# Performance work log

Measured on AMD Instinct MI355X. Metric: run time of the kernel, lower is better.

## Reference

```python
import jax, jax.numpy as jnp
import numpy as np
import math

B, T, C_EMB, H, M, P = 4, 8192, 1024, 16, 64, 8
D = C_EMB // H
L = int(math.log2(T // M)) - 1  # = 6 levels of coarse attention
SCALE_ATTN = True
NEG = -1e30


def setup_inputs() -> dict:
    key = jax.random.key(0)
    ks = jax.random.split(key, 4)
    x = jax.random.normal(ks[0], (B, T, C_EMB), jnp.float32)
    W_attn = jax.random.normal(ks[1], (C_EMB, 3 * C_EMB), jnp.float32) * (1.0 / math.sqrt(C_EMB))
    b_attn = jnp.zeros((3 * C_EMB,), jnp.float32)
    W_proj = jax.random.normal(ks[2], (C_EMB, C_EMB), jnp.float32) * (1.0 / math.sqrt(C_EMB))
    b_proj = jnp.zeros((C_EMB,), jnp.float32)
    return {"x": x, "W_attn": W_attn, "b_attn": b_attn, "W_proj": W_proj, "b_proj": b_proj}


def _shift(t, s):
    # shift blocks forward along axis 1 by s, zero-padding at the front
    pad = jnp.zeros_like(t[:, :s])
    return jnp.concatenate([pad, t[:, :-s]], axis=1)


def _fma_attention(q, k, v):
    # q, k, v: [BH, T, D]; q already scaled by 1/sqrt(D)
    BH = q.shape[0]
    # --- convolute(): avgpool downsampled K, V at each level ---
    Kls, Vls = [k], [v]
    for l in range(L):
        r = (M * 2 ** l) // P  # pool kernel = stride
        Kls.append(k.reshape(BH, T // r, r, D).mean(axis=2))
        Vls.append(v.reshape(BH, T // r, r, D).mean(axis=2))
    # --- stage1: banded QK at every level ---
    As = []
    # fine level 0: causal sliding window of M keys (j in [i-M+1, i])
    nb0 = T // M
    qb = q.reshape(BH, nb0, M, D)
    kb = k.reshape(BH, nb0, M, D)
    s_prev = jnp.einsum('bgqd,bgkd->bgqk', qb, _shift(kb, 1))
    s_self = jnp.einsum('bgqd,bgkd->bgqk', qb, kb)
    r_idx = jnp.arange(M)[:, None]
    c_idx = jnp.arange(M)[None, :]
    g_ok = (jnp.arange(nb0) >= 1)[None, :, None, None]
    s_prev = jnp.where((c_idx > r_idx) & g_ok, s_prev, NEG)
    s_self = jnp.where(c_idx <= r_idx, s_self, NEG)
    As.append(jnp.concatenate([s_prev, s_self], axis=-1).reshape(BH, T, 2 * M))
    # coarse levels l=1..L: query block (width w) attends to the P summaries of
    # each of the two preceding coarse blocks (causal, left-to-right)
    for l in range(1, L + 1):
        w = M * 2 ** (l - 1)
        nb = T // w
        qw = q.reshape(BH, nb, w, D)
        kc = Kls[l].reshape(BH, nb, P, D)
        scores = []
        for s in (2, 1):
            sc = jnp.einsum('bgqd,bgpd->bgqp', qw, _shift(kc, s))
            ok = (jnp.arange(nb) >= s)[None, :, None, None]
            scores.append(jnp.where(ok, sc, NEG))
        As.append(jnp.concatenate(scores, axis=-1).reshape(BH, T, 2 * P))
    # --- fused multi-level softmax (shared max + shared normalizer) ---
    gmax = jnp.max(jnp.stack([a.max(axis=-1) for a in As], axis=-1), axis=-1)  # [BH, T]
    Es = [jnp.exp(a - gmax[..., None]) for a in As]
    scales = [1] + [((M * 2 ** (l - 1)) // P if SCALE_ATTN else 1) for l in range(1, L + 1)]
    denom = sum(float(s) * e.sum(axis=-1) for s, e in zip(scales, Es))[..., None]
    Cs = [float(s) * e / denom for s, e in zip(scales, Es)]
    # --- stage2: banded CV ---
    vb = v.reshape(BH, nb0, M, D)
    C0 = Cs[0].reshape(BH, nb0, M, 2 * M)
    out = (jnp.einsum('bgqk,bgkd->bgqd', C0[..., :M], _shift(vb, 1)) +
           jnp.einsum('bgqk,bgkd->bgqd', C0[..., M:], vb)).reshape(BH, T, D)
    for l in range(1, L + 1):
        w = M * 2 ** (l - 1)
        nb = T // w
        vc = Vls[l].reshape(BH, nb, P, D)
        Cl = Cs[l].reshape(BH, nb, w, 2 * P)
        ol = (jnp.einsum('bgqp,bgpd->bgqd', Cl[..., :P], _shift(vc, 2)) +
              jnp.einsum('bgqp,bgpd->bgqd', Cl[..., P:], _shift(vc, 1)))
        out = out + ol.reshape(BH, T, D)
    return out


def reference(x, W_attn, b_attn, W_proj, b_proj):
    Bx, Tx, Cx = x.shape
    qkv = x @ W_attn + b_attn
    q, k, v = jnp.split(qkv, 3, axis=-1)

    def heads(t):
        return t.reshape(Bx, Tx, H, D).transpose(0, 2, 1, 3).reshape(Bx * H, Tx, D)

    q = heads(q) / math.sqrt(D)
    o = _fma_attention(q, heads(k), heads(v))
    o = o.reshape(Bx, H, Tx, D).transpose(0, 2, 1, 3).reshape(Bx, Tx, Cx)
    return o @ W_proj + b_proj
```

## Files before the change

### kernel.cpp

```cpp
#include <hip/hip_runtime.h>
#include <hip/hip_bf16.h>
#include <stdint.h>


typedef float  f32x4  __attribute__((ext_vector_type(4)));
typedef __bf16 bf16x8 __attribute__((ext_vector_type(8)));
typedef unsigned short ushort8 __attribute__((ext_vector_type(8)));
typedef unsigned short ushort4v __attribute__((ext_vector_type(4)));
typedef unsigned uint4v __attribute__((ext_vector_type(4)));

__device__ __forceinline__ unsigned short f2bf(float f) {
  union { float f; unsigned u; } v; v.f = f;
  unsigned r = v.u + 0x7fffu + ((v.u >> 16) & 1u);
  return (unsigned short)(r >> 16);
}
__device__ __forceinline__ float bf2f(unsigned short s) {
  union { unsigned u; float f; } v; v.u = ((unsigned)s) << 16;
  return v.f;
}
__device__ __forceinline__ bf16x8 ld_bf8(const unsigned short* p) {
  return __builtin_bit_cast(bf16x8, *(const ushort8*)p);
}
__device__ __forceinline__ f32x4 mfma16(bf16x8 a, bf16x8 b, f32x4 c) {
  return __builtin_amdgcn_mfma_f32_16x16x32_bf16(a, b, c, 0, 0, 0);
}
__device__ __forceinline__ f32x4 zero4() {
  f32x4 z; z[0] = 0.f; z[1] = 0.f; z[2] = 0.f; z[3] = 0.f; return z;
}
__device__ __forceinline__ void gload16(const void* g, void* lds) {
  __builtin_amdgcn_global_load_lds(
      (const __attribute__((address_space(1))) void*)(uintptr_t)g,
      (__attribute__((address_space(3))) void*)(unsigned int)(uintptr_t)lds,
      16, 0, 0);
}

#define T_SEQ 8192
#define NPOOL 2016

#define SCHED0() __builtin_amdgcn_sched_barrier(0)
#define VMC(n)                                           \
  do {                                                   \
    SCHED0();                                            \
    asm volatile("s_waitcnt vmcnt(" #n ")" ::: "memory");\
    SCHED0();                                            \
  } while (0)

__global__ __launch_bounds__(256) void castx_k(const float* __restrict__ x,
                                               unsigned short* __restrict__ xb) {
  size_t i = ((size_t)blockIdx.x * 256 + threadIdx.x) * 8;
  float4 a = *(const float4*)(x + i);
  float4 b = *(const float4*)(x + i + 4);
  ushort8 o;
  o[0] = f2bf(a.x); o[1] = f2bf(a.y); o[2] = f2bf(a.z); o[3] = f2bf(a.w);
  o[4] = f2bf(b.x); o[5] = f2bf(b.y); o[6] = f2bf(b.z); o[7] = f2bf(b.w);
  *(ushort8*)(xb + i) = o;
}

__global__ __launch_bounds__(256) void transposeW_k(const float* __restrict__ w,
                                                    unsigned short* __restrict__ wt,
                                                    int R, int C) {
  __shared__ float tile[64 * 65];
  int cc = blockIdx.x, rc = blockIdx.y;
  int tid = threadIdx.x;
#pragma unroll
  for (int p = 0; p < 4; ++p) {
    int ci = p * 256 + tid;
    int r = ci >> 4, q4 = ci & 15;
    float4 v = *(const float4*)(w + (size_t)(rc * 64 + r) * C + cc * 64 + q4 * 4);
    tile[r * 65 + q4 * 4 + 0] = v.x;
    tile[r * 65 + q4 * 4 + 1] = v.y;
    tile[r * 65 + q4 * 4 + 2] = v.z;
    tile[r * 65 + q4 * 4 + 3] = v.w;
  }
  __syncthreads();
#pragma unroll
  for (int p = 0; p < 2; ++p) {
    int orow = p * 32 + (tid >> 3), tg = tid & 7;
    ushort8 ov;
#pragma unroll
    for (int i = 0; i < 8; ++i) ov[i] = f2bf(tile[(tg * 8 + i) * 65 + orow]);
    *(ushort8*)(wt + (size_t)(cc * 64 + orow) * R + rc * 64 + tg * 8) = ov;
  }
}

template<int NTILE_N, int EPI>
__global__ __launch_bounds__(512, 2) void gemm256(
    const unsigned short* __restrict__ A, const unsigned short* __restrict__ Bt,
    const float* __restrict__ bias,
    unsigned short* __restrict__ o0, unsigned short* __restrict__ o1,
    unsigned short* __restrict__ o2, float* __restrict__ fout) {
  extern __shared__ __align__(16) char smem[];
  const int K = 1024;
  const int nwg = 128 * NTILE_N;
  const int q = nwg >> 3;
  const int wg = ((int)blockIdx.x & 7) * q + ((int)blockIdx.x >> 3);
  const int tm = wg & 127, tn = wg >> 7;
  const int tid = threadIdx.x;
  const int wid = tid >> 6, lane = tid & 63;
  const int wm = wid >> 2, wn = wid & 3;
  const int lr = lane & 15, lg = lane >> 4;

  const int srow = tid >> 2;
  const int sseg = (tid & 3) ^ ((tid >> 3) & 3);
  const unsigned short* aSrc = A + (size_t)(tm * 256 + srow) * K + sseg * 8;
  const unsigned short* bSrc = Bt + (size_t)(tn * 256 + srow) * K + sseg * 8;
  const unsigned ldsT = (unsigned)tid * 16;

  const unsigned psel = (unsigned)((lg ^ ((lr >> 1) & 3)) * 16);
  const unsigned aBase = (unsigned)(wm * 8192 + lr * 64) + psel;
  const unsigned bBase = (unsigned)(16384 + wn * 4096 + lr * 64) + psel;

  f32x4 acc[8][4];
#pragma unroll
  for (int i = 0; i < 8; ++i)
#pragma unroll
    for (int j = 0; j < 4; ++j) acc[i][j] = zero4();

  bf16x8 rA0[4], rA1[4], rB0[4], rB1[4];

  auto SB = [&]() {
    SCHED0();
    __builtin_amdgcn_s_barrier();
    SCHED0();
  };
  auto stage2 = [&](int coffShorts, unsigned slotB) {
#pragma unroll
    for (int pass = 0; pass < 2; ++pass) {
      gload16(aSrc + (size_t)pass * 128 * K + coffShorts,
              smem + slotB + pass * 8192 + ldsT);
      gload16(bSrc + (size_t)pass * 128 * K + coffShorts,
              smem + slotB + 16384 + pass * 8192 + ldsT);
    }
  };
  auto rdA = [&](bf16x8 (&dst)[4], unsigned slotB, int ih) {
    const char* p = smem + slotB + aBase + ih * 4096;
#pragma unroll
    for (int ii = 0; ii < 4; ++ii)
      dst[ii] = ld_bf8((const unsigned short*)(p + ii * 1024));
  };
  auto rdB = [&](bf16x8 (&dst)[4], unsigned slotB) {
    const char* p = smem + slotB + bBase;
#pragma unroll
    for (int j = 0; j < 4; ++j)
      dst[j] = ld_bf8((const unsigned short*)(p + j * 1024));
  };
  auto cluster = [&](int rb, bf16x8 (&a)[4], bf16x8 (&b)[4]) {
    __builtin_amdgcn_s_setprio(1);
#pragma unroll
    for (int ii = 0; ii < 4; ++ii)
#pragma unroll
      for (int j = 0; j < 4; ++j)
        acc[rb + ii][j] = mfma16(b[j], a[ii], acc[rb + ii][j]);
    __builtin_amdgcn_s_setprio(0);
  };

  stage2(0, 0u);
  stage2(32, 32768u);
  stage2(64, 65536u);
  stage2(96, 98304u);
  VMC(12);
  SB();
  rdA(rA0, 0u, 0);
  rdB(rB0, 0u);

  for (int t = 0; t < 16; ++t) {
    const unsigned s0  = (unsigned)((2 * t) & 3) * 32768u;
    const unsigned s1  = (unsigned)((2 * t + 1) & 3) * 32768u;
    const unsigned sn0 = (unsigned)((2 * t + 2) & 3) * 32768u;
    rdA(rA1, s0, 1);
    if (t < 15) { VMC(8); } else { VMC(0); }
    SB();
    cluster(0, rA0, rB0);
    if (t < 14) stage2((t + 2) * 64, s0);
    rdA(rA0, s1, 0);
    rdB(rB1, s1);
    SB();
    cluster(4, rA1, rB0);
    rdA(rA1, s1, 1);
    if (t < 14) { VMC(8); } else if (t == 14) { VMC(4); }
    SB();
    cluster(0, rA0, rB1);
    if (t < 14) stage2((t + 2) * 64 + 32, s1);
    if (t < 15) { rdA(rA0, sn0, 0); rdB(rB0, sn0); }
    SB();
    cluster(4, rA1, rB1);
  }

  const int mBase = tm * 256 + wm * 128;
  const int nBase = tn * 256 + wn * 64;
  if (EPI == 0) {
    const int region = nBase >> 10, nn = nBase & 1023, hh = nn >> 6;
    unsigned short* dst = region == 0 ? o0 : (region == 1 ? o1 : o2);
#pragma unroll
    for (int j = 0; j < 4; ++j) {
      const int d0 = (nn & 63) + j * 16 + lg * 4;
      const float4 bv = *(const float4*)(bias + nBase + j * 16 + lg * 4);
#pragma unroll
      for (int i = 0; i < 8; ++i) {
        const int m = mBase + i * 16 + lr;
        const int bb = m >> 13, tq = m & 8191;
        ushort4v pk;
        pk[0] = f2bf(acc[i][j][0] + bv.x);
        pk[1] = f2bf(acc[i][j][1] + bv.y);
        pk[2] = f2bf(acc[i][j][2] + bv.z);
        pk[3] = f2bf(acc[i][j][3] + bv.w);
        *(ushort4v*)(dst + (((size_t)(bb * 16 + hh)) * T_SEQ + tq) * 64 + d0) = pk;
      }
    }
  } else {
#pragma unroll
    for (int j = 0; j < 4; ++j) {
      const int n0 = nBase + j * 16 + lg * 4;
      const float4 bv = *(const float4*)(bias + n0);
#pragma unroll
      for (int i = 0; i < 8; ++i) {
        const int m = mBase + i * 16 + lr;
        float4 ov;
        ov.x = acc[i][j][0] + bv.x;
        ov.y = acc[i][j][1] + bv.y;
        ov.z = acc[i][j][2] + bv.z;
        ov.w = acc[i][j][3] + bv.w;
        *(float4*)(fout + (size_t)m * 1024 + n0) = ov;
      }
    }
  }
}

__global__ __launch_bounds__(256) void transposeV_k(const unsigned short* __restrict__ v,
                                                    unsigned short* __restrict__ vt) {
  __shared__ float tile[64 * 65];
  int tc = blockIdx.x, bh = blockIdx.y;
  int tid = threadIdx.x;
#pragma unroll
  for (int p = 0; p < 2; ++p) {
    int r = p * 32 + (tid >> 3), cg = tid & 7;
    ushort8 u = *(const ushort8*)(v + ((size_t)bh * T_SEQ + (size_t)tc * 64 + r) * 64 + cg * 8);
#pragma unroll
    for (int i = 0; i < 8; ++i) tile[r * 65 + cg * 8 + i] = bf2f(u[i]);
  }
  __syncthreads();
#pragma unroll
  for (int p = 0; p < 2; ++p) {
    int dd = p * 32 + (tid >> 3), tg = tid & 7;
    ushort8 ov;
#pragma unroll
    for (int i = 0; i < 8; ++i) ov[i] = f2bf(tile[(tg * 8 + i) * 65 + dd]);
    *(ushort8*)(vt + ((size_t)bh * 64 + dd) * T_SEQ + (size_t)tc * 64 + tg * 8) = ov;
  }
}

__global__ __launch_bounds__(256) void poolK_k(const unsigned short* __restrict__ kin,
                                               unsigned short* __restrict__ kpool) {
  __shared__ float buf[64 * 65];
  int chunk = blockIdx.x, bh = blockIdx.y;
  int tid = threadIdx.x;
  int cg = tid & 7, orow = tid >> 3;
  float s[8];
#pragma unroll
  for (int i = 0; i < 8; ++i) s[i] = 0.f;
  const unsigned short* base =
      kin + ((size_t)bh * T_SEQ + chunk * 256 + orow * 8) * 64 + cg * 8;
#pragma unroll
  for (int rr = 0; rr < 8; ++rr) {
    ushort8 v = *(const ushort8*)(base + (size_t)rr * 64);
#pragma unroll
    for (int i = 0; i < 8; ++i) s[i] += bf2f(v[i]);
  }
  unsigned short* kp = kpool + (size_t)bh * NPOOL * 64;
  {
    ushort8 ov;
#pragma unroll
    for (int i = 0; i < 8; ++i) {
      s[i] *= 0.125f;
      ov[i] = f2bf(s[i]);
      buf[orow * 65 + cg * 8 + i] = s[i];
    }
    *(ushort8*)(kp + ((size_t)(chunk * 32 + orow)) * 64 + cg * 8) = ov;
  }
  __syncthreads();
  int srcR = 0, dstR = 32;
#pragma unroll
  for (int lvl = 2; lvl <= 6; ++lvl) {
    int rows = 32 >> (lvl - 1);
    int off = 2048 - (2048 >> (lvl - 1));
    if (orow < rows) {
      ushort8 ov;
      float tv[8];
#pragma unroll
      for (int i = 0; i < 8; ++i) {
        tv[i] = 0.5f * (buf[(srcR + 2 * orow) * 65 + cg * 8 + i] +
                        buf[(srcR + 2 * orow + 1) * 65 + cg * 8 + i]);
        ov[i] = f2bf(tv[i]);
      }
      *(ushort8*)(kp + ((size_t)(off + chunk * rows + orow)) * 64 + cg * 8) = ov;
#pragma unroll
      for (int i = 0; i < 8; ++i) buf[(dstR + orow) * 65 + cg * 8 + i] = tv[i];
    }
    __syncthreads();
    srcR = dstR;
    dstR += rows;
  }
}

__global__ __launch_bounds__(256) void poolV_k(const unsigned short* __restrict__ vt,
                                               unsigned short* __restrict__ vtpool) {
  __shared__ float buf[1024 + 512 + 256 + 128 + 64];
  int d = blockIdx.x, bh = blockIdx.y;
  int tid = threadIdx.x;
  const unsigned short* src = vt + ((size_t)bh * 64 + d) * T_SEQ;
  unsigned short* dst = vtpool + ((size_t)bh * 64 + d) * NPOOL;
#pragma unroll
  for (int p = 0; p < 4; ++p) {
    int oi = p * 256 + tid;
    ushort8 v = *(const ushort8*)(src + (size_t)oi * 8);
    float s = 0.f;
#pragma unroll
    for (int i = 0; i < 8; ++i) s += bf2f(v[i]);
    s *= 0.125f;
    dst[oi] = f2bf(s);
    buf[oi] = s;
  }
  __syncthreads();
  float* b1 = buf; float* b2 = buf + 1024;
#pragma unroll
  for (int p = 0; p < 2; ++p) {
    int oi = p * 256 + tid;
    float s = 0.5f * (b1[2 * oi] + b1[2 * oi + 1]);
    dst[1024 + oi] = f2bf(s);
    b2[oi] = s;
  }
  __syncthreads();
  float* b3 = b2 + 512;
  {
    float s = 0.5f * (b2[2 * tid] + b2[2 * tid + 1]);
    dst[1536 + tid] = f2bf(s);
    b3[tid] = s;
  }
  __syncthreads();
  float* b4 = b3 + 256;
  if (tid < 128) {
    float s = 0.5f * (b3[2 * tid] + b3[2 * tid + 1]);
    dst[1792 + tid] = f2bf(s);
    b4[tid] = s;
  }
  __syncthreads();
  float* b5 = b4 + 128;
  if (tid < 64) {
    float s = 0.5f * (b4[2 * tid] + b4[2 * tid + 1]);
    dst[1920 + tid] = f2bf(s);
    b5[tid] = s;
  }
  __syncthreads();
  if (tid < 32) {
    float s = 0.5f * (b5[2 * tid] + b5[2 * tid + 1]);
    dst[1984 + tid] = f2bf(s);
  }
}

__global__ __launch_bounds__(256) void attn_k(const unsigned short* __restrict__ q,
                                              const unsigned short* __restrict__ k,
                                              const unsigned short* __restrict__ kpool,
                                              const unsigned short* __restrict__ vt,
                                              const unsigned short* __restrict__ vtpool,
                                              unsigned short* __restrict__ o) {
  const int g = blockIdx.x;
  const int bh = blockIdx.y;
  const int tid = threadIdx.x;
  const int w = tid >> 6, l = tid & 63;
  const int lr = l & 15, lg = l >> 4;
  __shared__ unsigned short KV[224 * 64];

  const size_t qoff = ((size_t)bh * T_SEQ + (size_t)g * 64 + w * 16 + lr) * 64 + lg * 8;
  bf16x8 aq0 = ld_bf8(q + qoff);
  bf16x8 aq1 = ld_bf8(q + qoff + 32);
  SCHED0();

  const int krow = tid >> 3;
  const int kseg = tid & 7;
#pragma unroll
  for (int p = 0; p < 7; ++p) {
    const int row = p * 32 + krow;
    const unsigned short* src;
    if (row < 128) {
      int t0 = (g - 1) * 64 + row;
      if (t0 < 0) t0 = 0;
      src = k + ((size_t)bh * T_SEQ + t0) * 64;
    } else {
      const int pr = row - 128;
      const int lvl0 = pr >> 4;
      const int off = 2048 - (2048 >> lvl0);
      const int gl = g >> lvl0;
      int st = (gl - 2) * 8 + (pr & 15);
      if (st < 0) st = 0;
      src = kpool + ((size_t)bh * NPOOL + off + st) * 64;
    }
    gload16(src + (kseg ^ (row & 7)) * 8,
            ((char*)KV) + p * 4096 + (unsigned)tid * 16);
  }
  SCHED0();

  const int vr = tid >> 2;
  const int vg = tid & 3;
  const int vswz = vg ^ ((vr >> 1) & 3);
  ushort8 vstg[7];
#pragma unroll
  for (int s = 0; s < 7; ++s) {
    const int colsh = s * 32 + vswz * 8;
    const unsigned short* src;
    if (colsh < 128) {
      int t0 = (g - 1) * 64 + colsh;
      if (t0 < 0) t0 = 0;
      src = vt + ((size_t)bh * 64 + vr) * T_SEQ + t0;
    } else {
      const int c = colsh - 128;
      const int lvl = c >> 4;
      const int off = 2048 - (2048 >> lvl);
      const int gl = g >> lvl;
      int start = (gl - 2) * 8 + (c & 15);
      if (start < 0) start = 0;
      src = vtpool + ((size_t)bh * 64 + vr) * NPOOL + off + start;
    }
    vstg[s] = *(const ushort8*)src;
  }
  SCHED0();
  asm volatile("s_waitcnt vmcnt(7)" ::: "memory");
  SCHED0();
  __builtin_amdgcn_s_barrier();
  SCHED0();

  f32x4 S[14];
#pragma unroll
  for (int ct = 0; ct < 14; ++ct) S[ct] = zero4();
#pragma unroll
  for (int ct = 0; ct < 14; ++ct) {
    const int row = ct * 16 + lr;
    const unsigned short* kr = KV + row * 64;
    const int sw = row & 7;
    S[ct] = mfma16(ld_bf8(kr + (lg ^ sw) * 8), aq0, S[ct]);
    S[ct] = mfma16(ld_bf8(kr + ((lg + 4) ^ sw) * 8), aq1, S[ct]);
  }
  SCHED0();
  __builtin_amdgcn_s_barrier();
  SCHED0();

#pragma unroll
  for (int s = 0; s < 7; ++s)
    *(ushort8*)&KV[s * 2048 + vr * 32 + vg * 8] = vstg[s];

  const float NEGF = -1e30f;
  const int qq = w * 16 + lr;
#pragma unroll
  for (int ct = 0; ct < 14; ++ct) {
#pragma unroll
    for (int e = 0; e < 4; ++e) {
      float s = S[ct][e] * 0.125f;
      bool valid;
      if (ct < 8) {
        int kk = ct * 16 + lg * 4 + e;
        valid = (kk > qq) && (kk <= qq + 64) && ((g >= 1) || (kk >= 64));
      } else {
        int lvl = ct - 7;
        int gl = g >> (lvl - 1);
        valid = gl >= ((lg < 2) ? 2 : 1);
      }
      S[ct][e] = valid ? s : NEGF;
    }
  }
  float mx = S[0][0];
#pragma unroll
  for (int ct = 0; ct < 14; ++ct)
#pragma unroll
    for (int e = 0; e < 4; ++e) mx = fmaxf(mx, S[ct][e]);
  mx = fmaxf(mx, __shfl_xor(mx, 16));
  mx = fmaxf(mx, __shfl_xor(mx, 32));
  float sum = 0.f;
#pragma unroll
  for (int ct = 0; ct < 14; ++ct) {
    const float sc = (ct < 8) ? 1.0f : (float)(8 << (ct - 8));
#pragma unroll
    for (int e = 0; e < 4; ++e) {
      float ev = sc * __expf(S[ct][e] - mx);
      S[ct][e] = ev;
      sum += ev;
    }
  }
  sum += __shfl_xor(sum, 16);
  sum += __shfl_xor(sum, 32);
  const float invd = 1.0f / sum;

  unsigned pw[14][2];
#pragma unroll
  for (int ct = 0; ct < 14; ++ct) {
    float p0 = S[ct][0] * invd, p1 = S[ct][1] * invd;
    float p2 = S[ct][2] * invd, p3 = S[ct][3] * invd;
    asm("v_cvt_pk_bf16_f32 %0, %1, %2" : "=v"(pw[ct][0]) : "v"(p0), "v"(p1));
    asm("v_cvt_pk_bf16_f32 %0, %1, %2" : "=v"(pw[ct][1]) : "v"(p2), "v"(p3));
  }

  const int src0 = lr + ((lg & 1) << 5);
  const int src1 = src0 + 16;
  const bool odd = (lg & 2) != 0;
  bf16x8 paf[7];
#pragma unroll
  for (int kc = 0; kc < 7; ++kc) {
    unsigned we0 = __shfl((int)pw[2 * kc][0], src0);
    unsigned we1 = __shfl((int)pw[2 * kc][1], src0);
    unsigned we2 = __shfl((int)pw[2 * kc][0], src1);
    unsigned we3 = __shfl((int)pw[2 * kc][1], src1);
    unsigned wo0 = __shfl((int)pw[2 * kc + 1][0], src0);
    unsigned wo1 = __shfl((int)pw[2 * kc + 1][1], src0);
    unsigned wo2 = __shfl((int)pw[2 * kc + 1][0], src1);
    unsigned wo3 = __shfl((int)pw[2 * kc + 1][1], src1);
    uint4v fw;
    fw[0] = odd ? wo0 : we0;
    fw[1] = odd ? wo1 : we1;
    fw[2] = odd ? wo2 : we2;
    fw[3] = odd ? wo3 : we3;
    paf[kc] = __builtin_bit_cast(bf16x8, fw);
  }
  __syncthreads();

  f32x4 O[4];
#pragma unroll
  for (int c2 = 0; c2 < 4; ++c2) O[c2] = zero4();
#pragma unroll
  for (int kc = 0; kc < 7; ++kc) {
#pragma unroll
    for (int c2 = 0; c2 < 4; ++c2) {
      const int row = c2 * 16 + lr;
      bf16x8 vb = ld_bf8(&KV[kc * 2048 + row * 32 + ((lg ^ ((lr >> 1) & 3)) * 8)]);
      O[c2] = mfma16(paf[kc], vb, O[c2]);
    }
  }
  const int bb = bh >> 4, hh = bh & 15;
#pragma unroll
  for (int c2 = 0; c2 < 4; ++c2) {
    int d = c2 * 16 + lr;
#pragma unroll
    for (int e = 0; e < 4; ++e) {
      int t = g * 64 + w * 16 + lg * 4 + e;
      o[((size_t)bb * T_SEQ + t) * 1024 + hh * 64 + d] = f2bf(O[c2][e]);
    }
  }
}

extern "C" void kernel_launch(void* const* d_in, const int* in_sizes, int n_in,
                              void* d_out, int out_size, void* d_ws, size_t ws_size,
                              hipStream_t stream) {
  const float* x  = (const float*)d_in[0];
  const float* Wa = (const float*)d_in[1];
  const float* ba = (const float*)d_in[2];
  const float* Wp = (const float*)d_in[3];
  const float* bp = (const float*)d_in[4];
  float* out = (float*)d_out;
  char* ws = (char*)d_ws;
  const size_t MB = 1024 * 1024;

  unsigned short* xb  = (unsigned short*)(ws);
  unsigned short* qb  = (unsigned short*)(ws + 64 * MB);
  unsigned short* kb  = (unsigned short*)(ws + 128 * MB);
  unsigned short* vb  = (unsigned short*)(ws + 192 * MB);
  unsigned short* vt  = (unsigned short*)(ws + 256 * MB);
  unsigned short* wat = (unsigned short*)(ws + 320 * MB);
  unsigned short* wpt = (unsigned short*)(ws + 326 * MB);
  unsigned short* kpool  = xb;
  unsigned short* vtpool = (unsigned short*)(ws + 32 * MB);

  hipFuncSetAttribute((const void*)gemm256<12, 0>,
                      hipFuncAttributeMaxDynamicSharedMemorySize, 131072);
  hipFuncSetAttribute((const void*)gemm256<4, 1>,
                      hipFuncAttributeMaxDynamicSharedMemorySize, 131072);

  castx_k<<<16384, 256, 0, stream>>>(x, xb);
  transposeW_k<<<dim3(48, 16), 256, 0, stream>>>(Wa, wat, 1024, 3072);
  transposeW_k<<<dim3(16, 16), 256, 0, stream>>>(Wp, wpt, 1024, 1024);
  gemm256<12, 0><<<1536, 512, 131072, stream>>>(xb, wat, ba, qb, kb, vb, nullptr);
  transposeV_k<<<dim3(128, 64), 256, 0, stream>>>(vb, vt);
  poolK_k<<<dim3(32, 64), 256, 0, stream>>>(kb, kpool);
  poolV_k<<<dim3(64, 64), 256, 0, stream>>>(vt, vtpool);
  attn_k<<<dim3(128, 64), 256, 0, stream>>>(qb, kb, kpool, vt, vtpool, vb);
  gemm256<4, 1><<<512, 512, 131072, stream>>>(vb, wpt, bp, nullptr, nullptr, nullptr, out);
}
```

Baseline: 506.3 us.

## Restructure GEMM main loop into 3-stage split A/B prefetch with two barriers per cluster

```diff
diff --git a/kernel.cpp b/kernel.cpp
--- a/kernel.cpp
+++ b/kernel.cpp
@@ -42,6 +42,11 @@
   do {                                                   \
     SCHED0();                                            \
     asm volatile("s_waitcnt vmcnt(" #n ")" ::: "memory");\
+    SCHED0();                                            \
+  } while (0)
+#define LGKM0()                                          \
+  do {                                                   \
+    asm volatile("s_waitcnt lgkmcnt(0)" ::: "memory");   \
     SCHED0();                                            \
   } while (0)
 
@@ -118,19 +123,22 @@
 
   bf16x8 rA0[4], rA1[4], rB0[4], rB1[4];
 
-  auto SB = [&]() {
+  auto BAR = [&]() {
     SCHED0();
     __builtin_amdgcn_s_barrier();
     SCHED0();
   };
-  auto stage2 = [&](int coffShorts, unsigned slotB) {
-#pragma unroll
-    for (int pass = 0; pass < 2; ++pass) {
+  auto stageA2 = [&](int coffShorts, unsigned slotB) {
+#pragma unroll
+    for (int pass = 0; pass < 2; ++pass)
       gload16(aSrc + (size_t)pass * 128 * K + coffShorts,
               smem + slotB + pass * 8192 + ldsT);
+  };
+  auto stageB2 = [&](int coffShorts, unsigned slotB) {
+#pragma unroll
+    for (int pass = 0; pass < 2; ++pass)
       gload16(bSrc + (size_t)pass * 128 * K + coffShorts,
               smem + slotB + 16384 + pass * 8192 + ldsT);
-    }
   };
   auto rdA = [&](bf16x8 (&dst)[4], unsigned slotB, int ih) {
     const char* p = smem + slotB + aBase + ih * 4096;
@@ -144,7 +152,7 @@
     for (int j = 0; j < 4; ++j)
       dst[j] = ld_bf8((const unsigned short*)(p + j * 1024));
   };
-  auto cluster = [&](int rb, bf16x8 (&a)[4], bf16x8 (&b)[4]) {
+  auto cl16 = [&](int rb, bf16x8 (&a)[4], bf16x8 (&b)[4]) {
     __builtin_amdgcn_s_setprio(1);
 #pragma unroll
     for (int ii = 0; ii < 4; ++ii)
@@ -154,36 +162,45 @@
     __builtin_amdgcn_s_setprio(0);
   };
 
-  stage2(0, 0u);
-  stage2(32, 32768u);
-  stage2(64, 65536u);
-  stage2(96, 98304u);
-  VMC(12);
-  SB();
-  rdA(rA0, 0u, 0);
-  rdB(rB0, 0u);
+  stageA2(0, 0u);      stageB2(0, 0u);
+  stageA2(32, 32768u); stageB2(32, 32768u);
+  stageA2(64, 65536u); stageB2(64, 65536u);
+  VMC(8);
+  BAR();
 
   for (int t = 0; t < 16; ++t) {
-    const unsigned s0  = (unsigned)((2 * t) & 3) * 32768u;
-    const unsigned s1  = (unsigned)((2 * t + 1) & 3) * 32768u;
-    const unsigned sn0 = (unsigned)((2 * t + 2) & 3) * 32768u;
+    const unsigned s0 = (unsigned)((2 * t) & 3) * 32768u;
+    const unsigned s1 = (unsigned)((2 * t + 1) & 3) * 32768u;
+    const unsigned d0 = (unsigned)((2 * t + 3) & 3) * 32768u;
+    const unsigned d1 = (unsigned)((2 * t + 4) & 3) * 32768u;
+    if (t < 15) stageA2((2 * t + 3) * 32, d0);
+    rdA(rA0, s0, 0);
+    rdB(rB0, s0);
+    BAR();
+    LGKM0();
+    cl16(0, rA0, rB0);
+    BAR();
+    if (t < 15) { VMC(6); } else { VMC(0); }
+    if (t < 15) stageB2((2 * t + 3) * 32, d0);
     rdA(rA1, s0, 1);
-    if (t < 15) { VMC(8); } else { VMC(0); }
-    SB();
-    cluster(0, rA0, rB0);
-    if (t < 14) stage2((t + 2) * 64, s0);
+    BAR();
+    LGKM0();
+    cl16(4, rA1, rB0);
+    BAR();
+    if (t < 14) stageA2((2 * t + 4) * 32, d1);
     rdA(rA0, s1, 0);
     rdB(rB1, s1);
-    SB();
-    cluster(4, rA1, rB0);
+    BAR();
+    LGKM0();
+    cl16(0, rA0, rB1);
+    BAR();
+    if (t < 14) { VMC(6); } else if (t == 14) { VMC(4); }
+    if (t < 14) stageB2((2 * t + 4) * 32, d1);
     rdA(rA1, s1, 1);
-    if (t < 14) { VMC(8); } else if (t == 14) { VMC(4); }
-    SB();
-    cluster(0, rA0, rB1);
-    if (t < 14) stage2((t + 2) * 64 + 32, s1);
-    if (t < 15) { rdA(rA0, sn0, 0); rdB(rB0, sn0); }
-    SB();
-    cluster(4, rA1, rB1);
+    BAR();
+    LGKM0();
+    cl16(4, rA1, rB1);
+    BAR();
   }
 
   const int mBase = tm * 256 + wm * 128;
@@ -193,7 +210,7 @@
     unsigned short* dst = region == 0 ? o0 : (region == 1 ? o1 : o2);
 #pragma unroll
     for (int j = 0; j < 4; ++j) {
-      const int d0 = (nn & 63) + j * 16 + lg * 4;
+      const int d0c = (nn & 63) + j * 16 + lg * 4;
       const float4 bv = *(const float4*)(bias + nBase + j * 16 + lg * 4);
 #pragma unroll
       for (int i = 0; i < 8; ++i) {
@@ -204,7 +221,7 @@
         pk[1] = f2bf(acc[i][j][1] + bv.y);
         pk[2] = f2bf(acc[i][j][2] + bv.z);
         pk[3] = f2bf(acc[i][j][3] + bv.w);
-        *(ushort4v*)(dst + (((size_t)(bb * 16 + hh)) * T_SEQ + tq) * 64 + d0) = pk;
+        *(ushort4v*)(dst + (((size_t)(bb * 16 + hh)) * T_SEQ + tq) * 64 + d0c) = pk;
       }
     }
   } else {
```

Result: no change. 511.6 us (+1.1%).
